# Optimization experiments

Measured on AMD Instinct MI355X. Metric: run time of the kernel, lower is better.

Reference implementation:

```python
import jax, jax.numpy as jnp
import numpy as np

D_IN = 1024
D_OUT = 1024
NUM_HEADS = 16
HEAD_DIM = D_OUT // NUM_HEADS
EPS = 1e-6
POW = 16.0


def setup_inputs() -> dict:
    key = jax.random.key(0)
    ks = jax.random.split(key, 6)
    s = 1.0 / np.sqrt(D_IN)
    x = jax.random.normal(ks[0], (2, 2048, D_IN), dtype=jnp.float32)
    Wq = jax.random.uniform(ks[1], (D_OUT, D_IN), jnp.float32, -s, s)
    Wk = jax.random.uniform(ks[2], (D_OUT, D_IN), jnp.float32, -s, s)
    Wv = jax.random.uniform(ks[3], (D_OUT, D_IN), jnp.float32, -s, s)
    Wo = jax.random.uniform(ks[4], (D_OUT, D_OUT), jnp.float32, -s, s)
    bo = jax.random.uniform(ks[5], (D_OUT,), jnp.float32, -s, s)
    return {"x": x, "Wq": Wq, "Wk": Wk, "Wv": Wv, "Wo": Wo, "bo": bo}


def _l2norm(t):
    # torch F.normalize: t / max(||t||, eps)
    n = jnp.sqrt(jnp.sum(t * t, axis=-1, keepdims=True))
    return t / jnp.maximum(n, EPS)


def reference(x, Wq, Wk, Wv, Wo, bo):
    B, T, _ = x.shape
    # project and split heads: [B, H, T, Dh]
    def heads(W):
        y = jnp.einsum('btd,od->bto', x, W)
        return y.reshape(B, T, NUM_HEADS, HEAD_DIM).transpose(0, 2, 1, 3)
    Q = _l2norm(heads(Wq))
    K = _l2norm(heads(Wk))
    V = heads(Wv)
    cos_sim = jnp.clip(jnp.einsum('bhtd,bhsd->bhts', Q, K), -0.999, 0.999)
    scores = 1.0 - jnp.arccos(cos_sim) / jnp.pi
    W = jnp.power(jnp.maximum(scores, EPS), POW)
    W = W / (jnp.sum(W, axis=-1, keepdims=True) + EPS)
    out = jnp.einsum('bhts,bhsd->bhtd', W, V)
    out = out.transpose(0, 2, 1, 3).reshape(B, T, D_OUT)
    return jnp.einsum('bto,po->btp', out, Wo) + bo
```

## Files before the change

### kernel.cpp

```cpp
#include <hip/hip_runtime.h>
#include <math.h>

constexpr int Dm   = 1024;
constexpr int NH   = 16;
constexpr int HD   = 64;
constexpr int Bb   = 2;
constexpr int Tt   = 2048;
constexpr int MTOT = Bb * Tt;
#define EPSF 1e-6f

typedef __attribute__((ext_vector_type(8))) short short8;
typedef __attribute__((ext_vector_type(4))) float f32x4;
typedef __attribute__((ext_vector_type(2))) float f32x2;

__device__ __forceinline__ ushort f2bf(float f) {
    union { float f; unsigned u; } v; v.f = f;
    unsigned r = (v.u + 0x7FFFu + ((v.u >> 16) & 1u)) >> 16;
    return (ushort)r;
}

__device__ __forceinline__ void gload16(const void* g, void* l) {
    __builtin_amdgcn_global_load_lds(
        (const __attribute__((address_space(1))) unsigned int*)g,
        (__attribute__((address_space(3))) unsigned int*)l,
        16, 0, 0);
}

__global__ __launch_bounds__(256)
void cvt_all(const float* __restrict__ x,  const float* __restrict__ wq,
             const float* __restrict__ wk, const float* __restrict__ wv,
             const float* __restrict__ wo,
             ushort* __restrict__ xb,  ushort* __restrict__ wqb,
             ushort* __restrict__ wkb, ushort* __restrict__ wvb,
             ushort* __restrict__ wob) {
    int i = blockIdx.x * 256 + threadIdx.x;
    const float* src; ushort* dst; int off;
    if (i < 1048576)      { src = x;  dst = xb;  off = i; }
    else if (i < 1310720) { src = wq; dst = wqb; off = i - 1048576; }
    else if (i < 1572864) { src = wk; dst = wkb; off = i - 1310720; }
    else if (i < 1835008) { src = wv; dst = wvb; off = i - 1572864; }
    else                  { src = wo; dst = wob; off = i - 1835008; }
    const float4 v = ((const float4*)src)[off];
    ushort4 o;
    o.x = f2bf(v.x); o.y = f2bf(v.y); o.z = f2bf(v.z); o.w = f2bf(v.w);
    ((ushort4*)dst)[off] = o;
}

template<bool OUTF32>
__device__ __forceinline__
void gemm_core(const ushort* __restrict__ A, const ushort* __restrict__ W,
               const float* __restrict__ bias, void* __restrict__ out,
               int m0, int n0, int N, int K, bool do_norm) {
    __shared__ ushort As[128 * 64];
    __shared__ ushort Bs[128 * 64];
    const int tid  = threadIdx.x;
    const int wave = tid >> 6, lane = tid & 63;
    const int quad = lane >> 4, l15 = lane & 15;
    const int wr = wave >> 1, wc = wave & 1;
    const int lr = lane >> 3;
    const int sc = (lane & 7) ^ lr;

    f32x4 acc[4][4] = {};
    const ushort* Ab = A + (size_t)(m0 + lr) * K + sc * 8;
    const ushort* Wb = W + (size_t)(n0 + lr) * K + sc * 8;

    for (int k0 = 0; k0 < K; k0 += 64) {
        #pragma unroll
        for (int i = 0; i < 4; i++) {
            const int rows8 = (wave * 4 + i) * 8;
            gload16(Ab + (size_t)rows8 * K + k0, &As[rows8 * 64]);
            gload16(Wb + (size_t)rows8 * K + k0, &Bs[rows8 * 64]);
        }
        __syncthreads();
        #pragma unroll
        for (int kh = 0; kh < 2; kh++) {
            short8 af[4];
            #pragma unroll
            for (int mi = 0; mi < 4; mi++) {
                const int row = wr * 64 + mi * 16 + l15;
                af[mi] = *(const short8*)&As[row * 64 + (((kh * 4 + quad) ^ (row & 7)) * 8)];
            }
            #pragma unroll
            for (int nj = 0; nj < 4; nj++) {
                const int row = wc * 64 + nj * 16 + l15;
                const short8 bf = *(const short8*)&Bs[row * 64 + (((kh * 4 + quad) ^ (row & 7)) * 8)];
                #pragma unroll
                for (int mi = 0; mi < 4; mi++)
                    acc[mi][nj] = __builtin_amdgcn_mfma_f32_16x16x32_bf16(af[mi], bf, acc[mi][nj], 0, 0, 0);
            }
        }
        __syncthreads();
    }

    #pragma unroll
    for (int mi = 0; mi < 4; mi++) {
        float inv[4] = {1.f, 1.f, 1.f, 1.f};
        if (!OUTF32 && do_norm) {
            #pragma unroll
            for (int r = 0; r < 4; r++) {
                float ss = 0.f;
                #pragma unroll
                for (int nj = 0; nj < 4; nj++) ss += acc[mi][nj][r] * acc[mi][nj][r];
                ss += __shfl_xor(ss, 1); ss += __shfl_xor(ss, 2);
                ss += __shfl_xor(ss, 4); ss += __shfl_xor(ss, 8);
                inv[r] = 1.f / fmaxf(sqrtf(ss), EPSF);
            }
        }
        #pragma unroll
        for (int nj = 0; nj < 4; nj++)
            #pragma unroll
            for (int r = 0; r < 4; r++) {
                const int row = m0 + wr * 64 + mi * 16 + quad * 4 + r;
                const int col = n0 + wc * 64 + nj * 16 + l15;
                if (OUTF32)
                    ((float*)out)[(size_t)row * N + col] = acc[mi][nj][r] + bias[col];
                else
                    ((ushort*)out)[(size_t)row * N + col] = f2bf(acc[mi][nj][r] * inv[r]);
            }
    }
}

__global__ __launch_bounds__(256)
void qkv_gemm(const ushort* __restrict__ xb,
              const ushort* __restrict__ wq, const ushort* __restrict__ wk,
              const ushort* __restrict__ wv,
              ushort* __restrict__ qb, ushort* __restrict__ kb,
              ushort* __restrict__ vb) {
    const int ny = blockIdx.y, sel = ny >> 3;
    const ushort* W = (sel == 0) ? wq : (sel == 1) ? wk : wv;
    ushort* out     = (sel == 0) ? qb : (sel == 1) ? kb : vb;
    gemm_core<false>(xb, W, nullptr, out, blockIdx.x * 128, (ny & 7) * 128,
                     Dm, Dm, sel < 2);
}

__global__ __launch_bounds__(256)
void out_gemm(const ushort* __restrict__ aob, const ushort* __restrict__ wob,
              const float* __restrict__ bias, float* __restrict__ out) {
    gemm_core<true>(aob, wob, bias, out, blockIdx.x * 128, blockIdx.y * 128,
                    Dm, Dm, false);
}

__global__ __launch_bounds__(256)
void vtranspose(const ushort* __restrict__ vb, ushort* __restrict__ vtb) {
    __shared__ ushort T[64][72];
    const int tid = threadIdx.x;
    const int s0 = blockIdx.x * 64, h = blockIdx.y, b = blockIdx.z;
    const size_t vtbase = (size_t)((b * NH + h) * HD) * Tt;
    for (int c = tid; c < 512; c += 256) {
        const int s = c >> 3, d0 = (c & 7) * 8;
        *(short8*)&T[s][d0] =
            *(const short8*)&vb[(size_t)(b * Tt + s0 + s) * Dm + h * HD + d0];
    }
    __syncthreads();
    for (int c = tid; c < 512; c += 256) {
        const int d = c >> 3, scol = (c & 7) * 8;
        short8 val;
        #pragma unroll
        for (int i = 0; i < 8; i++) val[i] = (short)T[scol + i][d];
        *(short8*)&vtb[vtbase + (size_t)d * Tt + s0 + scol] = val;
    }
}

__global__ __launch_bounds__(256)
void attn_kernel(const ushort* __restrict__ Qb, const ushort* __restrict__ Kb,
                 const ushort* __restrict__ Vtb, ushort* __restrict__ Ob) {
    __shared__ ushort Ks[2][64 * 64];
    __shared__ ushort Vs[2][64 * 64];
    __shared__ ushort Ws[128 * 64];
    const int tid  = threadIdx.x;
    const int wave = tid >> 6, lane = tid & 63;
    const int quad = lane >> 4, l15 = lane & 15;
    const int t0 = blockIdx.x * 128, h = blockIdx.y, b = blockIdx.z;

    short8 qf[2][2];
    #pragma unroll
    for (int mi = 0; mi < 2; mi++) {
        const size_t qrow =
            (size_t)(b * Tt + t0 + 32 * wave + 16 * mi + l15) * Dm + h * HD;
        qf[mi][0] = *(const short8*)&Qb[qrow + quad * 8];
        qf[mi][1] = *(const short8*)&Qb[qrow + 32 + quad * 8];
    }

    const size_t kbase  = (size_t)(b * Tt) * Dm + h * HD;
    const size_t vtbase = (size_t)((b * NH + h) * HD) * Tt;
    const int r0 = tid >> 3, ch0 = tid & 7;
    const ushort* kg = Kb  + kbase  + (size_t)r0 * Dm + ch0 * 8;
    const ushort* vg = Vtb + vtbase + (size_t)r0 * Tt + ch0 * 8;
    const int lsw0 = r0 * 64 + ((ch0 ^ (r0 & 7)) * 8);
    const int lsw1 = (r0 + 32) * 64 + ((ch0 ^ (r0 & 7)) * 8);

    f32x4 oacc[2][4] = {};
    f32x2 denp[2][4] = {};

    const f32x2 k3 = {-0.00596162f, -0.00596162f};
    const f32x2 k2 = { 0.02363680f,  0.02363680f};
    const f32x2 k1 = {-0.06751768f, -0.06751768f};
    const f32x2 k0 = { 0.49997415f,  0.49997415f};

    short8 pk0 = *(const short8*)kg;
    short8 pk1 = *(const short8*)(kg + (size_t)32 * Dm);
    short8 pv0 = *(const short8*)vg;
    short8 pv1 = *(const short8*)(vg + (size_t)32 * Tt);
    *(short8*)&Ks[0][lsw0] = pk0;  *(short8*)&Ks[0][lsw1] = pk1;
    *(short8*)&Vs[0][lsw0] = pv0;  *(short8*)&Vs[0][lsw1] = pv1;
    __syncthreads();

    for (int i = 0; i < 32; i++) {
        const int p = i & 1;
        if (i < 31) {
            const size_t sn = (size_t)(i + 1) * 64;
            pk0 = *(const short8*)(kg + sn * Dm);
            pk1 = *(const short8*)(kg + (sn + 32) * Dm);
            pv0 = *(const short8*)(vg + sn);
            pv1 = *(const short8*)(vg + sn + (size_t)32 * Tt);
        }

        f32x4 sf[2][4] = {};
        #pragma unroll
        for (int j = 0; j < 4; j++) {
            const int row = 16 * j + l15;
            const short8 kf0 = *(const short8*)&Ks[p][row * 64 + ((quad ^ (row & 7)) * 8)];
            const short8 kf1 = *(const short8*)&Ks[p][row * 64 + (((4 + quad) ^ (row & 7)) * 8)];
            #pragma unroll
            for (int mi = 0; mi < 2; mi++) {
                sf[mi][j] = __builtin_amdgcn_mfma_f32_16x16x32_bf16(qf[mi][0], kf0, sf[mi][j], 0, 0, 0);
                sf[mi][j] = __builtin_amdgcn_mfma_f32_16x16x32_bf16(qf[mi][1], kf1, sf[mi][j], 0, 0, 0);
            }
        }

        #pragma unroll
        for (int mi = 0; mi < 2; mi++)
            #pragma unroll
            for (int r = 0; r < 4; r++) {
                f32x2 ca, cb;
                ca.x = __builtin_amdgcn_fmed3f(sf[mi][0][r], -0.999f, 0.999f);
                ca.y = __builtin_amdgcn_fmed3f(sf[mi][1][r], -0.999f, 0.999f);
                cb.x = __builtin_amdgcn_fmed3f(sf[mi][2][r], -0.999f, 0.999f);
                cb.y = __builtin_amdgcn_fmed3f(sf[mi][3][r], -0.999f, 0.999f);
                f32x2 axa = {fabsf(ca.x), fabsf(ca.y)};
                f32x2 axb = {fabsf(cb.x), fabsf(cb.y)};
                f32x2 pa = __builtin_elementwise_fma(axa, k3, k2);
                f32x2 pb = __builtin_elementwise_fma(axb, k3, k2);
                pa = __builtin_elementwise_fma(pa, axa, k1);
                pb = __builtin_elementwise_fma(pb, axb, k1);
                pa = __builtin_elementwise_fma(pa, axa, k0);
                pb = __builtin_elementwise_fma(pb, axb, k0);
                f32x2 ta = 1.0f - axa, tb = 1.0f - axb;
                ta.x = __builtin_amdgcn_sqrtf(ta.x); ta.y = __builtin_amdgcn_sqrtf(ta.y);
                tb.x = __builtin_amdgcn_sqrtf(tb.x); tb.y = __builtin_amdgcn_sqrtf(tb.y);
                const f32x2 rpa = ta * pa, rpb = tb * pb;
                const f32x2 da = 0.5f - rpa, db = 0.5f - rpb;
                f32x2 csa = {__builtin_copysignf(da.x, ca.x), __builtin_copysignf(da.y, ca.y)};
                f32x2 csb = {__builtin_copysignf(db.x, cb.x), __builtin_copysignf(db.y, cb.y)};
                f32x2 wa = csa + 0.5f, wb = csb + 0.5f;
                wa *= wa; wa *= wa; wa *= wa; wa *= wa;
                wb *= wb; wb *= wb; wb *= wb; wb *= wb;
                denp[mi][r] += wa; denp[mi][r] += wb;
                const int wrow = 32 * wave + 16 * mi + quad * 4 + r;
                const int wb7 = wrow & 7;
                const int base = wrow * 64 + (l15 & 7);
                const int hc = l15 >> 3;
                Ws[base + (((hc)     ^ wb7) * 8)] = f2bf(wa.x);
                Ws[base + (((hc + 2) ^ wb7) * 8)] = f2bf(wa.y);
                Ws[base + (((hc + 4) ^ wb7) * 8)] = f2bf(wb.x);
                Ws[base + (((hc + 6) ^ wb7) * 8)] = f2bf(wb.y);
            }
        __syncthreads();

        short8 wf[2][2];
        #pragma unroll
        for (int mi = 0; mi < 2; mi++) {
            const int wrow = 32 * wave + 16 * mi + l15;
            wf[mi][0] = *(const short8*)&Ws[wrow * 64 + ((quad ^ (wrow & 7)) * 8)];
            wf[mi][1] = *(const short8*)&Ws[wrow * 64 + (((4 + quad) ^ (wrow & 7)) * 8)];
        }
        #pragma unroll
        for (int j = 0; j < 4; j++) {
            const int vrow = 16 * j + l15;
            const short8 vf0 = *(const short8*)&Vs[p][vrow * 64 + ((quad ^ (vrow & 7)) * 8)];
            const short8 vf1 = *(const short8*)&Vs[p][vrow * 64 + (((4 + quad) ^ (vrow & 7)) * 8)];
            #pragma unroll
            for (int mi = 0; mi < 2; mi++) {
                oacc[mi][j] = __builtin_amdgcn_mfma_f32_16x16x32_bf16(wf[mi][0], vf0, oacc[mi][j], 0, 0, 0);
                oacc[mi][j] = __builtin_amdgcn_mfma_f32_16x16x32_bf16(wf[mi][1], vf1, oacc[mi][j], 0, 0, 0);
            }
        }
        if (i < 31) {
            *(short8*)&Ks[1 - p][lsw0] = pk0;  *(short8*)&Ks[1 - p][lsw1] = pk1;
            *(short8*)&Vs[1 - p][lsw0] = pv0;  *(short8*)&Vs[1 - p][lsw1] = pv1;
        }
        __syncthreads();
    }

    #pragma unroll
    for (int mi = 0; mi < 2; mi++) {
        float den[4];
        #pragma unroll
        for (int r = 0; r < 4; r++) {
            float d = denp[mi][r].x + denp[mi][r].y;
            d += __shfl_xor(d, 1); d += __shfl_xor(d, 2);
            d += __shfl_xor(d, 4); d += __shfl_xor(d, 8);
            den[r] = d;
        }
        const size_t obase =
            (size_t)(b * Tt + t0 + 32 * wave + 16 * mi + quad * 4) * Dm + h * HD + l15;
        #pragma unroll
        for (int j = 0; j < 4; j++)
            #pragma unroll
            for (int r = 0; r < 4; r++)
                Ob[obase + (size_t)r * Dm + 16 * j] =
                    f2bf(oacc[mi][j][r] / (den[r] + EPSF));
    }
}

extern "C" void kernel_launch(void* const* d_in, const int* in_sizes, int n_in,
                              void* d_out, int out_size, void* d_ws, size_t ws_size,
                              hipStream_t stream) {
    const float* x  = (const float*)d_in[0];
    const float* Wq = (const float*)d_in[1];
    const float* Wk = (const float*)d_in[2];
    const float* Wv = (const float*)d_in[3];
    const float* Wo = (const float*)d_in[4];
    const float* bo = (const float*)d_in[5];
    float* out = (float*)d_out;

    ushort* ws = (ushort*)d_ws;
    const size_t M1 = 1u << 20;
    ushort* xb  = ws;
    ushort* wqb = ws + 4 * M1;
    ushort* wkb = ws + 5 * M1;
    ushort* wvb = ws + 6 * M1;
    ushort* wob = ws + 7 * M1;
    ushort* qb  = ws + 8 * M1;
    ushort* kb  = ws + 12 * M1;
    ushort* vb  = ws + 16 * M1;
    ushort* vtb = ws + 20 * M1;
    ushort* aob = ws + 24 * M1;

    cvt_all<<<8192, 256, 0, stream>>>(x, Wq, Wk, Wv, Wo, xb, wqb, wkb, wvb, wob);
    qkv_gemm<<<dim3(MTOT / 128, 24), 256, 0, stream>>>(xb, wqb, wkb, wvb, qb, kb, vb);
    vtranspose<<<dim3(Tt / 64, NH, Bb), 256, 0, stream>>>(vb, vtb);
    attn_kernel<<<dim3(Tt / 128, NH, Bb), 256, 0, stream>>>(qb, kb, vtb, aob);
    out_gemm<<<dim3(MTOT / 128, Dm / 128), 256, 0, stream>>>(aob, wob, bo, out);
}
```

Measured before the change: 242.4 us.

## Fuse V transpose into QKV GEMM epilogue and halve attention query tile

The QKV GEMM now writes V directly in transposed per-head layout from its epilogue, which removes the separate vtranspose kernel and its round trip through global memory. The attention kernel is also changed from 128 to 64 query rows per block, one 16-row tile per wave, so twice as many blocks are launched, each with smaller register and LDS footprints. In exchange, every K/V tile is loaded from global memory twice as often, and the transposed V stores are 8-byte strided writes.

```diff
diff --git a/kernel.cpp b/kernel.cpp
--- a/kernel.cpp
+++ b/kernel.cpp
@@ -50,7 +50,7 @@
 __device__ __forceinline__
 void gemm_core(const ushort* __restrict__ A, const ushort* __restrict__ W,
                const float* __restrict__ bias, void* __restrict__ out,
-               int m0, int n0, int N, int K, bool do_norm) {
+               int m0, int n0, int N, int K, int mode) {
     __shared__ ushort As[128 * 64];
     __shared__ ushort Bs[128 * 64];
     const int tid  = threadIdx.x;
@@ -92,10 +92,28 @@
         __syncthreads();
     }
 
+    if (!OUTF32 && mode == 2) {
+        #pragma unroll
+        for (int mi = 0; mi < 4; mi++) {
+            const int t  = m0 + wr * 64 + mi * 16 + quad * 4;
+            const int bb = t >> 11, tl = t & 2047;
+            #pragma unroll
+            for (int nj = 0; nj < 4; nj++) {
+                const int n = n0 + wc * 64 + nj * 16 + l15;
+                const int hh = n >> 6, dd = n & 63;
+                uint2 pk;
+                pk.x = (unsigned)f2bf(acc[mi][nj][0]) | ((unsigned)f2bf(acc[mi][nj][1]) << 16);
+                pk.y = (unsigned)f2bf(acc[mi][nj][2]) | ((unsigned)f2bf(acc[mi][nj][3]) << 16);
+                *(uint2*)&((ushort*)out)[(size_t)((bb * NH + hh) * HD + dd) * Tt + tl] = pk;
+            }
+        }
+        return;
+    }
+
     #pragma unroll
     for (int mi = 0; mi < 4; mi++) {
         float inv[4] = {1.f, 1.f, 1.f, 1.f};
-        if (!OUTF32 && do_norm) {
+        if (!OUTF32 && mode == 1) {
             #pragma unroll
             for (int r = 0; r < 4; r++) {
                 float ss = 0.f;
@@ -125,40 +143,19 @@
               const ushort* __restrict__ wq, const ushort* __restrict__ wk,
               const ushort* __restrict__ wv,
               ushort* __restrict__ qb, ushort* __restrict__ kb,
-              ushort* __restrict__ vb) {
+              ushort* __restrict__ vtb) {
     const int ny = blockIdx.y, sel = ny >> 3;
     const ushort* W = (sel == 0) ? wq : (sel == 1) ? wk : wv;
-    ushort* out     = (sel == 0) ? qb : (sel == 1) ? kb : vb;
+    ushort* out     = (sel == 0) ? qb : (sel == 1) ? kb : vtb;
     gemm_core<false>(xb, W, nullptr, out, blockIdx.x * 128, (ny & 7) * 128,
-                     Dm, Dm, sel < 2);
+                     Dm, Dm, (sel < 2) ? 1 : 2);
 }
 
 __global__ __launch_bounds__(256)
 void out_gemm(const ushort* __restrict__ aob, const ushort* __restrict__ wob,
               const float* __restrict__ bias, float* __restrict__ out) {
     gemm_core<true>(aob, wob, bias, out, blockIdx.x * 128, blockIdx.y * 128,
-                    Dm, Dm, false);
-}
-
-__global__ __launch_bounds__(256)
-void vtranspose(const ushort* __restrict__ vb, ushort* __restrict__ vtb) {
-    __shared__ ushort T[64][72];
-    const int tid = threadIdx.x;
-    const int s0 = blockIdx.x * 64, h = blockIdx.y, b = blockIdx.z;
-    const size_t vtbase = (size_t)((b * NH + h) * HD) * Tt;
-    for (int c = tid; c < 512; c += 256) {
-        const int s = c >> 3, d0 = (c & 7) * 8;
-        *(short8*)&T[s][d0] =
-            *(const short8*)&vb[(size_t)(b * Tt + s0 + s) * Dm + h * HD + d0];
-    }
-    __syncthreads();
-    for (int c = tid; c < 512; c += 256) {
-        const int d = c >> 3, scol = (c & 7) * 8;
-        short8 val;
-        #pragma unroll
-        for (int i = 0; i < 8; i++) val[i] = (short)T[scol + i][d];
-        *(short8*)&vtb[vtbase + (size_t)d * Tt + s0 + scol] = val;
-    }
+                    Dm, Dm, 0);
 }
 
 __global__ __launch_bounds__(256)
@@ -166,20 +163,15 @@
                  const ushort* __restrict__ Vtb, ushort* __restrict__ Ob) {
     __shared__ ushort Ks[2][64 * 64];
     __shared__ ushort Vs[2][64 * 64];
-    __shared__ ushort Ws[128 * 64];
+    __shared__ ushort Ws[64 * 64];
     const int tid  = threadIdx.x;
     const int wave = tid >> 6, lane = tid & 63;
     const int quad = lane >> 4, l15 = lane & 15;
-    const int t0 = blockIdx.x * 128, h = blockIdx.y, b = blockIdx.z;
-
-    short8 qf[2][2];
-    #pragma unroll
-    for (int mi = 0; mi < 2; mi++) {
-        const size_t qrow =
-            (size_t)(b * Tt + t0 + 32 * wave + 16 * mi + l15) * Dm + h * HD;
-        qf[mi][0] = *(const short8*)&Qb[qrow + quad * 8];
-        qf[mi][1] = *(const short8*)&Qb[qrow + 32 + quad * 8];
-    }
+    const int t0 = blockIdx.x * 64, h = blockIdx.y, b = blockIdx.z;
+
+    const size_t qrow = (size_t)(b * Tt + t0 + 16 * wave + l15) * Dm + h * HD;
+    const short8 qf0 = *(const short8*)&Qb[qrow + quad * 8];
+    const short8 qf1 = *(const short8*)&Qb[qrow + 32 + quad * 8];
 
     const size_t kbase  = (size_t)(b * Tt) * Dm + h * HD;
     const size_t vtbase = (size_t)((b * NH + h) * HD) * Tt;
@@ -189,8 +181,8 @@
     const int lsw0 = r0 * 64 + ((ch0 ^ (r0 & 7)) * 8);
     const int lsw1 = (r0 + 32) * 64 + ((ch0 ^ (r0 & 7)) * 8);
 
-    f32x4 oacc[2][4] = {};
-    f32x2 denp[2][4] = {};
+    f32x4 oacc[4] = {};
+    f32x2 denp[4] = {};
 
     const f32x2 k3 = {-0.00596162f, -0.00596162f};
     const f32x2 k2 = { 0.02363680f,  0.02363680f};
@@ -215,75 +207,63 @@
             pv1 = *(const short8*)(vg + sn + (size_t)32 * Tt);
         }
 
-        f32x4 sf[2][4] = {};
+        f32x4 sf[4] = {};
         #pragma unroll
         for (int j = 0; j < 4; j++) {
             const int row = 16 * j + l15;
             const short8 kf0 = *(const short8*)&Ks[p][row * 64 + ((quad ^ (row & 7)) * 8)];
             const short8 kf1 = *(const short8*)&Ks[p][row * 64 + (((4 + quad) ^ (row & 7)) * 8)];
-            #pragma unroll
-            for (int mi = 0; mi < 2; mi++) {
-                sf[mi][j] = __builtin_amdgcn_mfma_f32_16x16x32_bf16(qf[mi][0], kf0, sf[mi][j], 0, 0, 0);
-                sf[mi][j] = __builtin_amdgcn_mfma_f32_16x16x32_bf16(qf[mi][1], kf1, sf[mi][j], 0, 0, 0);
-            }
-        }
-
-        #pragma unroll
-        for (int mi = 0; mi < 2; mi++)
-            #pragma unroll
-            for (int r = 0; r < 4; r++) {
-                f32x2 ca, cb;
-                ca.x = __builtin_amdgcn_fmed3f(sf[mi][0][r], -0.999f, 0.999f);
-                ca.y = __builtin_amdgcn_fmed3f(sf[mi][1][r], -0.999f, 0.999f);
-                cb.x = __builtin_amdgcn_fmed3f(sf[mi][2][r], -0.999f, 0.999f);
-                cb.y = __builtin_amdgcn_fmed3f(sf[mi][3][r], -0.999f, 0.999f);
-                f32x2 axa = {fabsf(ca.x), fabsf(ca.y)};
-                f32x2 axb = {fabsf(cb.x), fabsf(cb.y)};
-                f32x2 pa = __builtin_elementwise_fma(axa, k3, k2);
-                f32x2 pb = __builtin_elementwise_fma(axb, k3, k2);
-                pa = __builtin_elementwise_fma(pa, axa, k1);
-                pb = __builtin_elementwise_fma(pb, axb, k1);
-                pa = __builtin_elementwise_fma(pa, axa, k0);
-                pb = __builtin_elementwise_fma(pb, axb, k0);
-                f32x2 ta = 1.0f - axa, tb = 1.0f - axb;
-                ta.x = __builtin_amdgcn_sqrtf(ta.x); ta.y = __builtin_amdgcn_sqrtf(ta.y);
-                tb.x = __builtin_amdgcn_sqrtf(tb.x); tb.y = __builtin_amdgcn_sqrtf(tb.y);
-                const f32x2 rpa = ta * pa, rpb = tb * pb;
-                const f32x2 da = 0.5f - rpa, db = 0.5f - rpb;
-                f32x2 csa = {__builtin_copysignf(da.x, ca.x), __builtin_copysignf(da.y, ca.y)};
-                f32x2 csb = {__builtin_copysignf(db.x, cb.x), __builtin_copysignf(db.y, cb.y)};
-                f32x2 wa = csa + 0.5f, wb = csb + 0.5f;
-                wa *= wa; wa *= wa; wa *= wa; wa *= wa;
-                wb *= wb; wb *= wb; wb *= wb; wb *= wb;
-                denp[mi][r] += wa; denp[mi][r] += wb;
-                const int wrow = 32 * wave + 16 * mi + quad * 4 + r;
-                const int wb7 = wrow & 7;
-                const int base = wrow * 64 + (l15 & 7);
-                const int hc = l15 >> 3;
-                Ws[base + (((hc)     ^ wb7) * 8)] = f2bf(wa.x);
-                Ws[base + (((hc + 2) ^ wb7) * 8)] = f2bf(wa.y);
-                Ws[base + (((hc + 4) ^ wb7) * 8)] = f2bf(wb.x);
-                Ws[base + (((hc + 6) ^ wb7) * 8)] = f2bf(wb.y);
-            }
+            sf[j] = __builtin_amdgcn_mfma_f32_16x16x32_bf16(qf0, kf0, sf[j], 0, 0, 0);
+            sf[j] = __builtin_amdgcn_mfma_f32_16x16x32_bf16(qf1, kf1, sf[j], 0, 0, 0);
+        }
+
+        #pragma unroll
+        for (int r = 0; r < 4; r++) {
+            f32x2 ca, cb;
+            ca.x = __builtin_amdgcn_fmed3f(sf[0][r], -0.999f, 0.999f);
+            ca.y = __builtin_amdgcn_fmed3f(sf[1][r], -0.999f, 0.999f);
+            cb.x = __builtin_amdgcn_fmed3f(sf[2][r], -0.999f, 0.999f);
+            cb.y = __builtin_amdgcn_fmed3f(sf[3][r], -0.999f, 0.999f);
+            f32x2 axa = {fabsf(ca.x), fabsf(ca.y)};
+            f32x2 axb = {fabsf(cb.x), fabsf(cb.y)};
+            f32x2 pa = __builtin_elementwise_fma(axa, k3, k2);
+            f32x2 pb = __builtin_elementwise_fma(axb, k3, k2);
+            pa = __builtin_elementwise_fma(pa, axa, k1);
+            pb = __builtin_elementwise_fma(pb, axb, k1);
+            pa = __builtin_elementwise_fma(pa, axa, k0);
+            pb = __builtin_elementwise_fma(pb, axb, k0);
+            f32x2 ta = 1.0f - axa, tb = 1.0f - axb;
+            ta.x = __builtin_amdgcn_sqrtf(ta.x); ta.y = __builtin_amdgcn_sqrtf(ta.y);
+            tb.x = __builtin_amdgcn_sqrtf(tb.x); tb.y = __builtin_amdgcn_sqrtf(tb.y);
+            const f32x2 rpa = ta * pa, rpb = tb * pb;
+            const f32x2 da = 0.5f - rpa, db = 0.5f - rpb;
+            f32x2 csa = {__builtin_copysignf(da.x, ca.x), __builtin_copysignf(da.y, ca.y)};
+            f32x2 csb = {__builtin_copysignf(db.x, cb.x), __builtin_copysignf(db.y, cb.y)};
+            f32x2 wa = csa + 0.5f, wb = csb + 0.5f;
+            wa *= wa; wa *= wa; wa *= wa; wa *= wa;
+            wb *= wb; wb *= wb; wb *= wb; wb *= wb;
+            denp[r] += wa; denp[r] += wb;
+            const int wrow = 16 * wave + quad * 4 + r;
+            const int wb7 = wrow & 7;
+            const int base = wrow * 64 + (l15 & 7);
+            const int hc = l15 >> 3;
+            Ws[base + (((hc)     ^ wb7) * 8)] = f2bf(wa.x);
+            Ws[base + (((hc + 2) ^ wb7) * 8)] = f2bf(wa.y);
+            Ws[base + (((hc + 4) ^ wb7) * 8)] = f2bf(wb.x);
+            Ws[base + (((hc + 6) ^ wb7) * 8)] = f2bf(wb.y);
+        }
         __syncthreads();
 
-        short8 wf[2][2];
-        #pragma unroll
-        for (int mi = 0; mi < 2; mi++) {
-            const int wrow = 32 * wave + 16 * mi + l15;
-            wf[mi][0] = *(const short8*)&Ws[wrow * 64 + ((quad ^ (wrow & 7)) * 8)];
-            wf[mi][1] = *(const short8*)&Ws[wrow * 64 + (((4 + quad) ^ (wrow & 7)) * 8)];
-        }
+        const int wrow = 16 * wave + l15;
+        const short8 wf0 = *(const short8*)&Ws[wrow * 64 + ((quad ^ (wrow & 7)) * 8)];
+        const short8 wf1 = *(const short8*)&Ws[wrow * 64 + (((4 + quad) ^ (wrow & 7)) * 8)];
         #pragma unroll
         for (int j = 0; j < 4; j++) {
             const int vrow = 16 * j + l15;
             const short8 vf0 = *(const short8*)&Vs[p][vrow * 64 + ((quad ^ (vrow & 7)) * 8)];
             const short8 vf1 = *(const short8*)&Vs[p][vrow * 64 + (((4 + quad) ^ (vrow & 7)) * 8)];
-            #pragma unroll
-            for (int mi = 0; mi < 2; mi++) {
-                oacc[mi][j] = __builtin_amdgcn_mfma_f32_16x16x32_bf16(wf[mi][0], vf0, oacc[mi][j], 0, 0, 0);
-                oacc[mi][j] = __builtin_amdgcn_mfma_f32_16x16x32_bf16(wf[mi][1], vf1, oacc[mi][j], 0, 0, 0);
-            }
+            oacc[j] = __builtin_amdgcn_mfma_f32_16x16x32_bf16(wf0, vf0, oacc[j], 0, 0, 0);
+            oacc[j] = __builtin_amdgcn_mfma_f32_16x16x32_bf16(wf1, vf1, oacc[j], 0, 0, 0);
         }
         if (i < 31) {
             *(short8*)&Ks[1 - p][lsw0] = pk0;  *(short8*)&Ks[1 - p][lsw1] = pk1;
@@ -292,25 +272,21 @@
         __syncthreads();
     }
 
+    float den[4];
     #pragma unroll
-    for (int mi = 0; mi < 2; mi++) {
-        float den[4];
-        #pragma unroll
-        for (int r = 0; r < 4; r++) {
-            float d = denp[mi][r].x + denp[mi][r].y;
-            d += __shfl_xor(d, 1); d += __shfl_xor(d, 2);
-            d += __shfl_xor(d, 4); d += __shfl_xor(d, 8);
-            den[r] = d;
-        }
-        const size_t obase =
-            (size_t)(b * Tt + t0 + 32 * wave + 16 * mi + quad * 4) * Dm + h * HD + l15;
-        #pragma unroll
-        for (int j = 0; j < 4; j++)
-            #pragma unroll
-            for (int r = 0; r < 4; r++)
-                Ob[obase + (size_t)r * Dm + 16 * j] =
-                    f2bf(oacc[mi][j][r] / (den[r] + EPSF));
-    }
+    for (int r = 0; r < 4; r++) {
+        float d = denp[r].x + denp[r].y;
+        d += __shfl_xor(d, 1); d += __shfl_xor(d, 2);
+        d += __shfl_xor(d, 4); d += __shfl_xor(d, 8);
+        den[r] = d;
+    }
+    const size_t obase =
+        (size_t)(b * Tt + t0 + 16 * wave + quad * 4) * Dm + h * HD + l15;
+    #pragma unroll
+    for (int j = 0; j < 4; j++)
+        #pragma unroll
+        for (int r = 0; r < 4; r++)
+            Ob[obase + (size_t)r * Dm + 16 * j] = f2bf(oacc[j][r] / (den[r] + EPSF));
 }
 
 extern "C" void kernel_launch(void* const* d_in, const int* in_sizes, int n_in,
@@ -333,13 +309,11 @@
     ushort* wob = ws + 7 * M1;
     ushort* qb  = ws + 8 * M1;
     ushort* kb  = ws + 12 * M1;
-    ushort* vb  = ws + 16 * M1;
-    ushort* vtb = ws + 20 * M1;
-    ushort* aob = ws + 24 * M1;
+    ushort* vtb = ws + 16 * M1;
+    ushort* aob = ws + 20 * M1;
 
     cvt_all<<<8192, 256, 0, stream>>>(x, Wq, Wk, Wv, Wo, xb, wqb, wkb, wvb, wob);
-    qkv_gemm<<<dim3(MTOT / 128, 24), 256, 0, stream>>>(xb, wqb, wkb, wvb, qb, kb, vb);
-    vtranspose<<<dim3(Tt / 64, NH, Bb), 256, 0, stream>>>(vb, vtb);
-    attn_kernel<<<dim3(Tt / 128, NH, Bb), 256, 0, stream>>>(qb, kb, vtb, aob);
+    qkv_gemm<<<dim3(MTOT / 128, 24), 256, 0, stream>>>(xb, wqb, wkb, wvb, qb, kb, vtb);
+    attn_kernel<<<dim3(Tt / 64, NH, Bb), 256, 0, stream>>>(qb, kb, vtb, aob);
     out_gemm<<<dim3(MTOT / 128, Dm / 128), 256, 0, stream>>>(aob, wob, bo, out);
 }
```

Result: faster. 236.4 us (-2.5%).
